# Kernel tuning notes

Measured on AMD Instinct MI355X. Metric: run time of the kernel, lower is better.

## Reference

```python
import jax, jax.numpy as jnp
import numpy as np

N = 512
D = 512
# static upper-triangle pair indices (i < j)
_II, _JJ = np.triu_indices(N, k=1)
_II = jnp.asarray(_II)
_JJ = jnp.asarray(_JJ)


def setup_inputs() -> dict:
    key = jax.random.key(0)
    ks = jax.random.split(key, 9)
    s = 0.02
    return {
        'features': jax.random.normal(ks[0], (N, D), dtype=jnp.float32),
        # relation_classifier: Linear(2D->D), Linear(D->10)
        'cw1': jax.random.normal(ks[1], (2 * D, D), dtype=jnp.float32) * s,
        'cb1': jnp.zeros((D,), dtype=jnp.float32),
        'cw2': jax.random.normal(ks[2], (D, 10), dtype=jnp.float32) * s,
        'cb2': jnp.zeros((10,), dtype=jnp.float32),
        # relation_strength_calc: Linear(2D->D//2), Linear(D//2->1)
        'sw1': jax.random.normal(ks[3], (2 * D, D // 2), dtype=jnp.float32) * s,
        'sb1': jnp.zeros((D // 2,), dtype=jnp.float32),
        'sw2': jax.random.normal(ks[4], (D // 2, 1), dtype=jnp.float32) * s,
        'sb2': jnp.zeros((1,), dtype=jnp.float32),
    }


def reference(features, cw1, cb1, cw2, cb2, sw1, sb1, sw2, sb2):
    # cat([f_i, f_j]) @ W == f_i @ W[:D] + f_j @ W[D:]  (linear-split trick)
    # precompute per-node projections once, then gather per pair
    c_a = features @ cw1[:D]   # [N, D]
    c_b = features @ cw1[D:]   # [N, D]
    s_a = features @ sw1[:D]   # [N, D//2]
    s_b = features @ sw1[D:]   # [N, D//2]

    # classifier path
    h = jax.nn.relu(c_a[_II] + c_b[_JJ] + cb1)          # [P, D]
    relation_types = jax.nn.log_softmax(h @ cw2 + cb2)   # [P, 10]
    most_likely_relations = jnp.argmax(relation_types, axis=-1)  # [P]

    # strength path
    hs = jax.nn.relu(s_a[_II] + s_b[_JJ] + sb1)          # [P, D//2]
    relation_strengths = jax.nn.sigmoid(hs @ sw2 + sb2)   # [P, 1]

    return relation_types, most_likely_relations, relation_strengths
```

## Files before the change

### kernel.cpp

```cpp
#include <hip/hip_runtime.h>
#include <math.h>

#define NN 512
#define DD 512
#define NPAIRS 130816
#define TYPES_OFF 0
#define ARGMAX_OFF 1308160
#define STRENGTH_OFF 1438976

#define GAP_THRESH 2.5e-4f


__device__ __forceinline__ void fma64_step4(
    const float4& a0, const float4& a1, const float4& a2, const float4& a3,
    const float4& b0, const float4& b1, const float4& b2, const float4& b3,
    double acc[4][4])
{
    const float av[4][4] = {{a0.x,a0.y,a0.z,a0.w},{a1.x,a1.y,a1.z,a1.w},
                            {a2.x,a2.y,a2.z,a2.w},{a3.x,a3.y,a3.z,a3.w}};
    const float bv[4][4] = {{b0.x,b0.y,b0.z,b0.w},{b1.x,b1.y,b1.z,b1.w},
                            {b2.x,b2.y,b2.z,b2.w},{b3.x,b3.y,b3.z,b3.w}};
    #pragma unroll
    for (int kk = 0; kk < 4; ++kk) {
        double bd0 = (double)bv[kk][0], bd1 = (double)bv[kk][1];
        double bd2 = (double)bv[kk][2], bd3 = (double)bv[kk][3];
        #pragma unroll
        for (int rr = 0; rr < 4; ++rr) {
            double ad = (double)av[rr][kk];
            acc[rr][0] = fma(ad, bd0, acc[rr][0]);
            acc[rr][1] = fma(ad, bd1, acc[rr][1]);
            acc[rr][2] = fma(ad, bd2, acc[rr][2]);
            acc[rr][3] = fma(ad, bd3, acc[rr][3]);
        }
    }
}

__device__ __forceinline__ void fma32_step4(
    const float4& a0, const float4& a1, const float4& a2, const float4& a3,
    const float4& b0, const float4& b1, const float4& b2, const float4& b3,
    float acc[4][4])
{
    const float av[4][4] = {{a0.x,a0.y,a0.z,a0.w},{a1.x,a1.y,a1.z,a1.w},
                            {a2.x,a2.y,a2.z,a2.w},{a3.x,a3.y,a3.z,a3.w}};
    const float bv[4][4] = {{b0.x,b0.y,b0.z,b0.w},{b1.x,b1.y,b1.z,b1.w},
                            {b2.x,b2.y,b2.z,b2.w},{b3.x,b3.y,b3.z,b3.w}};
    #pragma unroll
    for (int kk = 0; kk < 4; ++kk) {
        #pragma unroll
        for (int rr = 0; rr < 4; ++rr) {
            #pragma unroll
            for (int cc = 0; cc < 4; ++cc)
                acc[rr][cc] = fmaf(av[rr][kk], bv[kk][cc], acc[rr][cc]);
        }
    }
}

__global__ __launch_bounds__(256, 2) void proj_kernel(
    const float* __restrict__ F, const float* __restrict__ cw1,
    const float* __restrict__ sw1,
    const float* __restrict__ cb1, const float* __restrict__ sb1,
    double* __restrict__ ca0, double* __restrict__ ca1,
    double* __restrict__ ca2, double* __restrict__ ca3,
    double* __restrict__ cb0, double* __restrict__ cb1p,
    double* __restrict__ cb2p, double* __restrict__ cb3p,
    float* __restrict__ sa0, float* __restrict__ sa1,
    float* __restrict__ sb0, float* __restrict__ sbp1)
{
    const int t = threadIdx.x;
    const int w = t >> 6;
    const int lane = t & 63;
    const int mg = lane >> 4;
    const int nq = lane & 15;

    if (blockIdx.x < 512) {
        const int b  = blockIdx.x;
        const int z  = b & 3;
        const int nt = (b >> 2) & 15;
        const int mt = b >> 6;
        const int n  = nt * 64;
        const float* W = (n < 512) ? cw1 : cw1 + 512 * 512;
        const int n0   = (n < 512) ? n : n - 512;
        double* outp;
        if (n < 512) outp = (z == 0) ? ca0 : (z == 1) ? ca1 : (z == 2) ? ca2 : ca3;
        else         outp = (z == 0) ? cb0 : (z == 1) ? cb1p : (z == 2) ? cb2p : cb3p;
        const bool addbias = (z == 0) && (n < 512);

        const int row0 = mt * 64 + w * 16 + mg * 4;
        const int col0 = n0 + nq * 4;
        const float* pa = F + row0 * 512 + z * 128;
        const float* pb = W + (z * 128) * 512 + col0;

        double acc[4][4];
        #pragma unroll
        for (int rr = 0; rr < 4; ++rr)
            #pragma unroll
            for (int cc = 0; cc < 4; ++cc) acc[rr][cc] = 0.0;

        float4 a0 = *(const float4*)(pa);
        float4 a1 = *(const float4*)(pa + 512);
        float4 a2 = *(const float4*)(pa + 1024);
        float4 a3 = *(const float4*)(pa + 1536);
        float4 b0 = *(const float4*)(pb);
        float4 b1 = *(const float4*)(pb + 512);
        float4 b2 = *(const float4*)(pb + 1024);
        float4 b3 = *(const float4*)(pb + 1536);
        for (int s = 0; s < 31; ++s) {
            const float* npa = pa + (s + 1) * 4;
            float4 na0 = *(const float4*)(npa);
            float4 na1 = *(const float4*)(npa + 512);
            float4 na2 = *(const float4*)(npa + 1024);
            float4 na3 = *(const float4*)(npa + 1536);
            const float* nb = pb + (s + 1) * 2048;
            float4 nb0 = *(const float4*)(nb);
            float4 nb1 = *(const float4*)(nb + 512);
            float4 nb2 = *(const float4*)(nb + 1024);
            float4 nb3 = *(const float4*)(nb + 1536);
            fma64_step4(a0, a1, a2, a3, b0, b1, b2, b3, acc);
            a0 = na0; a1 = na1; a2 = na2; a3 = na3;
            b0 = nb0; b1 = nb1; b2 = nb2; b3 = nb3;
        }
        fma64_step4(a0, a1, a2, a3, b0, b1, b2, b3, acc);

        #pragma unroll
        for (int rr = 0; rr < 4; ++rr) {
            double v[4];
            #pragma unroll
            for (int cc = 0; cc < 4; ++cc) {
                v[cc] = acc[rr][cc];
                if (addbias) v[cc] += (double)cb1[col0 + cc];
            }
            double* dst = outp + (row0 + rr) * 512 + col0;
            *(double2*)(dst + 0) = make_double2(v[0], v[1]);
            *(double2*)(dst + 2) = make_double2(v[2], v[3]);
        }
    } else {
        const int sbk = blockIdx.x - 512;
        const int z  = sbk & 1;
        const int nt = (sbk >> 1) & 7;
        const int mt = sbk >> 4;
        const int n  = nt * 64;
        const float* W = (n < 256) ? sw1 : sw1 + 512 * 256;
        const int n0   = (n < 256) ? n : n - 256;
        float* outp    = (n < 256) ? (z ? sa1 : sa0) : (z ? sbp1 : sb0);
        const bool addbias = (z == 0) && (n < 256);

        const int row0 = mt * 64 + w * 16 + mg * 4;
        const int col0 = n0 + nq * 4;
        const float* pa = F + row0 * 512 + z * 256;
        const float* pb = W + (z * 256) * 256 + col0;

        float acc[4][4];
        #pragma unroll
        for (int rr = 0; rr < 4; ++rr)
            #pragma unroll
            for (int cc = 0; cc < 4; ++cc) acc[rr][cc] = 0.f;

        float4 a0 = *(const float4*)(pa);
        float4 a1 = *(const float4*)(pa + 512);
        float4 a2 = *(const float4*)(pa + 1024);
        float4 a3 = *(const float4*)(pa + 1536);
        float4 b0 = *(const float4*)(pb);
        float4 b1 = *(const float4*)(pb + 256);
        float4 b2 = *(const float4*)(pb + 512);
        float4 b3 = *(const float4*)(pb + 768);
        for (int s = 0; s < 63; ++s) {
            const float* npa = pa + (s + 1) * 4;
            float4 na0 = *(const float4*)(npa);
            float4 na1 = *(const float4*)(npa + 512);
            float4 na2 = *(const float4*)(npa + 1024);
            float4 na3 = *(const float4*)(npa + 1536);
            const float* nb = pb + (s + 1) * 1024;
            float4 nb0 = *(const float4*)(nb);
            float4 nb1 = *(const float4*)(nb + 256);
            float4 nb2 = *(const float4*)(nb + 512);
            float4 nb3 = *(const float4*)(nb + 768);
            fma32_step4(a0, a1, a2, a3, b0, b1, b2, b3, acc);
            a0 = na0; a1 = na1; a2 = na2; a3 = na3;
            b0 = nb0; b1 = nb1; b2 = nb2; b3 = nb3;
        }
        fma32_step4(a0, a1, a2, a3, b0, b1, b2, b3, acc);

        #pragma unroll
        for (int rr = 0; rr < 4; ++rr) {
            float4 v = make_float4(acc[rr][0], acc[rr][1], acc[rr][2], acc[rr][3]);
            if (addbias) {
                v.x += sb1[col0 + 0]; v.y += sb1[col0 + 1];
                v.z += sb1[col0 + 2]; v.w += sb1[col0 + 3];
            }
            *(float4*)(outp + (row0 + rr) * 256 + col0) = v;
        }
    }
}

__global__ __launch_bounds__(256) void combine_kernel(
    const double* __restrict__ ca0, const double* __restrict__ ca1,
    const double* __restrict__ ca2, const double* __restrict__ ca3,
    const double* __restrict__ cb0, const double* __restrict__ cb1p,
    const double* __restrict__ cb2p, const double* __restrict__ cb3p,
    const float* __restrict__ sa0, const float* __restrict__ sa1,
    const float* __restrict__ sb0, const float* __restrict__ sbp1,
    float* __restrict__ cfa, float* __restrict__ cfb,
    float* __restrict__ sfa, float* __restrict__ sfb)
{
    const int t = blockIdx.x * 256 + threadIdx.x;
    {
        const int e = 2 * t;
        double2 x0 = *(const double2*)(ca0 + e);
        double2 x1 = *(const double2*)(ca1 + e);
        double2 x2 = *(const double2*)(ca2 + e);
        double2 x3 = *(const double2*)(ca3 + e);
        *(float2*)(cfa + e) = make_float2(
            (float)((x0.x + x1.x) + (x2.x + x3.x)),
            (float)((x0.y + x1.y) + (x2.y + x3.y)));
        double2 y0 = *(const double2*)(cb0 + e);
        double2 y1 = *(const double2*)(cb1p + e);
        double2 y2 = *(const double2*)(cb2p + e);
        double2 y3 = *(const double2*)(cb3p + e);
        *(float2*)(cfb + e) = make_float2(
            (float)((y0.x + y1.x) + (y2.x + y3.x)),
            (float)((y0.y + y1.y) + (y2.y + y3.y)));
    }
    if (t < 65536) {
        const bool second = t >= 32768;
        const int e = (second ? (t - 32768) : t) * 4;
        const float* s0 = second ? sb0 : sa0;
        const float* s1 = second ? sbp1 : sa1;
        float* dst      = second ? sfb : sfa;
        float4 a = *(const float4*)(s0 + e);
        float4 b = *(const float4*)(s1 + e);
        *(float4*)(dst + e) = make_float4(a.x + b.x, a.y + b.y, a.z + b.z, a.w + b.w);
    }
}

__global__ __launch_bounds__(256, 4) void pair_kernel(
    const double* __restrict__ ca0, const double* __restrict__ ca1,
    const double* __restrict__ ca2, const double* __restrict__ ca3,
    const double* __restrict__ cb0, const double* __restrict__ cb1p,
    const double* __restrict__ cb2p, const double* __restrict__ cb3p,
    const float* __restrict__ cfa, const float* __restrict__ cfb,
    const float* __restrict__ sfa, const float* __restrict__ sfb,
    const float* __restrict__ cw2, const float* __restrict__ cb2,
    const float* __restrict__ sw2, const float* __restrict__ sb2,
    float* __restrict__ out)
{
    const int b = blockIdx.x;
    int bi = (int)floorf((129.0f - sqrtf(16641.0f - 8.0f * (float)b)) * 0.5f);
    while ((bi + 1) * (129 - (bi + 1)) / 2 <= b) ++bi;
    while (bi * (129 - bi) / 2 > b) --bi;
    const int bj = bi + (b - bi * (129 - bi) / 2);
    const int i0 = bi * 8, j0 = bj * 8;

    const int t = threadIdx.x;
    const int q  = t >> 6;
    const int qu = __builtin_amdgcn_readfirstlane(q);
    const int l = t & 63;
    const int pi = l >> 3, pj = l & 7;
    const int i = i0 + pi, j = j0 + pj;

    __shared__ __align__(16) float smem[8448];
    float* sA  = smem;
    float* sB  = smem + 4224;
    float* sSa = smem;
    float* sSb = smem + 2176;
    float* lgbuf = smem;
    float* stbuf = smem + 1920;

    #pragma unroll
    for (int u = 0; u < 4; ++u) {
        int idx = u * 256 + t;
        int kq  = idx & 15;
        int row = (idx >> 4) & 7;
        int qq  = (idx >> 7) & 3;
        int arr = idx >> 9;
        int off = (arr ? (j0 + row) : (i0 + row)) * 256 + qq * 64 + kq * 4;
        const float* src = arr ? sfb : sfa;
        float4 v = *(const float4*)(src + off);
        float* dst = (arr ? sSb : sSa) + (qq * 8 + row) * 68 + kq * 4;
        *(float4*)dst = v;
    }
    __syncthreads();
    float accs = 0.f;
    {
        const float* sw2q = sw2 + qu * 64;
        const float* ra = sSa + (q * 8 + pi) * 68;
        const float* rb = sSb + (q * 8 + pj) * 68;
        float p0 = 0.f, p1 = 0.f, p2 = 0.f, p3 = 0.f;
        for (int kk = 0; kk < 64; kk += 4) {
            float4 a4 = *(const float4*)(ra + kk);
            float4 b4 = *(const float4*)(rb + kk);
            p0 = fmaf(fmaxf(a4.x + b4.x, 0.f), sw2q[kk + 0], p0);
            p1 = fmaf(fmaxf(a4.y + b4.y, 0.f), sw2q[kk + 1], p1);
            p2 = fmaf(fmaxf(a4.z + b4.z, 0.f), sw2q[kk + 2], p2);
            p3 = fmaf(fmaxf(a4.w + b4.w, 0.f), sw2q[kk + 3], p3);
        }
        accs = (p0 + p1) + (p2 + p3);
    }
    __syncthreads();

    #pragma unroll
    for (int u = 0; u < 8; ++u) {
        int idx = u * 256 + t;
        int kq  = idx & 31;
        int row = (idx >> 5) & 7;
        int qq  = (idx >> 8) & 3;
        int arr = idx >> 10;
        int off = (arr ? (j0 + row) : (i0 + row)) * 512 + qq * 128 + kq * 4;
        const float* src = arr ? cfb : cfa;
        float4 v = *(const float4*)(src + off);
        float* dst = (arr ? sB : sA) + (qq * 8 + row) * 132 + kq * 4;
        *(float4*)dst = v;
    }
    __syncthreads();

    float lg[10];
    #pragma unroll
    for (int c = 0; c < 10; ++c) lg[c] = 0.f;
    {
        const float* ra = sA + (q * 8 + pi) * 132;
        const float* rb = sB + (q * 8 + pj) * 132;
        const float* wr = cw2 + qu * 1280;
        for (int kk = 0; kk < 128; kk += 4) {
            float4 ra4 = *(const float4*)(ra + kk);
            float4 rb4 = *(const float4*)(rb + kk);
            float h0 = fmaxf(ra4.x + rb4.x, 0.f);
            float h1 = fmaxf(ra4.y + rb4.y, 0.f);
            float h2 = fmaxf(ra4.z + rb4.z, 0.f);
            float h3 = fmaxf(ra4.w + rb4.w, 0.f);
            const float* w = wr + kk * 10;
            #pragma unroll
            for (int c = 0; c < 10; ++c) lg[c] = fmaf(h0, w[c], lg[c]);
            #pragma unroll
            for (int c = 0; c < 10; ++c) lg[c] = fmaf(h1, w[10 + c], lg[c]);
            #pragma unroll
            for (int c = 0; c < 10; ++c) lg[c] = fmaf(h2, w[20 + c], lg[c]);
            #pragma unroll
            for (int c = 0; c < 10; ++c) lg[c] = fmaf(h3, w[30 + c], lg[c]);
        }
    }

    __syncthreads();
    if (q > 0) {
        float* dst = lgbuf + ((q - 1) * 64 + l) * 10;
        #pragma unroll
        for (int c = 0; c < 10; ++c) dst[c] = lg[c];
        stbuf[(q - 1) * 64 + l] = accs;
    }
    __syncthreads();
    if (q == 0) {
        #pragma unroll
        for (int w = 0; w < 3; ++w) {
            const float* srcb = lgbuf + (w * 64 + l) * 10;
            #pragma unroll
            for (int c = 0; c < 10; ++c) lg[c] += srcb[c];
        }
        float st = accs + stbuf[l] + stbuf[64 + l] + stbuf[128 + l] + sb2[0];

        #pragma unroll
        for (int c = 0; c < 10; ++c) lg[c] += cb2[c];

        float mx = lg[0], mx2 = -3.0e38f; int am2 = 0;
        #pragma unroll
        for (int c = 1; c < 10; ++c) {
            if (lg[c] > mx) { mx2 = mx; mx = lg[c]; am2 = c; }
            else if (lg[c] > mx2) mx2 = lg[c];
        }

        unsigned long long m = __ballot((j > i) && (mx - mx2 < GAP_THRESH));
        while (m) {
            const int s = __ffsll((unsigned long long)m) - 1; m &= (m - 1);
            const int si = i0 + (s >> 3), sj = j0 + (s & 7);
            double part[10];
            #pragma unroll
            for (int c = 0; c < 10; ++c) part[c] = 0.0;
            const int kb = l * 8;
            #pragma unroll 2
            for (int kk = 0; kk < 8; ++kk) {
                const int k = kb + kk;
                const int ei = si * 512 + k, ej = sj * 512 + k;
                double va = (ca0[ei] + ca1[ei]) + (ca2[ei] + ca3[ei]);
                double vb = (cb0[ej] + cb1p[ej]) + (cb2p[ej] + cb3p[ej]);
                double h = fmax(va + vb, 0.0);
                const float* w = cw2 + k * 10;
                #pragma unroll
                for (int c = 0; c < 10; ++c) part[c] = fma(h, (double)w[c], part[c]);
            }
            #pragma unroll
            for (int off = 32; off > 0; off >>= 1) {
                #pragma unroll
                for (int c = 0; c < 10; ++c) part[c] += __shfl_xor(part[c], off, 64);
            }
            double bmx = part[0] + (double)cb2[0]; int ba = 0;
            #pragma unroll
            for (int c = 1; c < 10; ++c) {
                double v = part[c] + (double)cb2[c];
                if (v > bmx) { bmx = v; ba = c; }
            }
            if (l == s) am2 = ba;
        }

        float tf[10]; float ssum = 0.f;
        #pragma unroll
        for (int c = 0; c < 10; ++c) { tf[c] = lg[c] - mx; ssum += __expf(tf[c]); }
        float ls = __logf(ssum);

        if (j > i) {
            const int p = i * 511 - (i * (i - 1)) / 2 + (j - i - 1);
            float* tp = out + TYPES_OFF + p * 10;
            #pragma unroll
            for (int c = 0; c < 10; ++c) tp[c] = tf[c] - ls;
            out[ARGMAX_OFF + p] = (float)am2;
            out[STRENGTH_OFF + p] = 1.0f / (1.0f + __expf(-st));
        }
    }
}

extern "C" void kernel_launch(void* const* d_in, const int* in_sizes, int n_in,
                              void* d_out, int out_size, void* d_ws, size_t ws_size,
                              hipStream_t stream) {
    const float* F   = (const float*)d_in[0];
    const float* cw1 = (const float*)d_in[1];
    const float* cb1 = (const float*)d_in[2];
    const float* cw2 = (const float*)d_in[3];
    const float* cb2 = (const float*)d_in[4];
    const float* sw1 = (const float*)d_in[5];
    const float* sb1 = (const float*)d_in[6];
    const float* sw2 = (const float*)d_in[7];
    const float* sb2 = (const float*)d_in[8];
    float* out = (float*)d_out;

    char* ws = (char*)d_ws;
    double* ca0  = (double*)(ws);
    double* ca1  = (double*)(ws + 2097152);
    double* ca2  = (double*)(ws + 4194304);
    double* ca3  = (double*)(ws + 6291456);
    double* cb0  = (double*)(ws + 8388608);
    double* cb1p = (double*)(ws + 10485760);
    double* cb2p = (double*)(ws + 12582912);
    double* cb3p = (double*)(ws + 14680064);
    float*  sa0  = (float*)(ws + 16777216);
    float*  sa1  = (float*)(ws + 17301504);
    float*  sb0  = (float*)(ws + 17825792);
    float*  sbp1 = (float*)(ws + 18350080);
    float*  cfa  = (float*)(ws + 18874368);
    float*  cfb  = (float*)(ws + 19922944);
    float*  sfa  = (float*)(ws + 20971520);
    float*  sfb  = (float*)(ws + 21495808);

    hipLaunchKernelGGL(proj_kernel, dim3(640), dim3(256), 0, stream,
                       F, cw1, sw1, cb1, sb1,
                       ca0, ca1, ca2, ca3, cb0, cb1p, cb2p, cb3p,
                       sa0, sa1, sb0, sbp1);
    hipLaunchKernelGGL(combine_kernel, dim3(512), dim3(256), 0, stream,
                       ca0, ca1, ca2, ca3, cb0, cb1p, cb2p, cb3p,
                       sa0, sa1, sb0, sbp1, cfa, cfb, sfa, sfb);
    hipLaunchKernelGGL(pair_kernel, dim3(2080), dim3(256), 0, stream,
                       ca0, ca1, ca2, ca3, cb0, cb1p, cb2p, cb3p,
                       cfa, cfb, sfa, sfb, cw2, cb2, sw2, sb2, out);
}
```

Baseline: 145.2 us.

## Enlarge projection register tile to 8x4 and double split-K partitions

Each projection thread now computes an 8x4 output tile instead of 4x4, which raises FMA work per loaded A/B value. The K dimension is split into 8 partitions for the fp64 classifier path and 4 for the fp32 strength path, up from 4 and 2, so the block count stays at 640. The partial buffers are packed into one contiguous array, and the combine kernel and the pair kernel's near-tie fallback now sum 8 fp64 partials instead of 4. The cost is twice the partial-sum write and read traffic, more register pressure from the fp64 accumulators, and extra loads in the fallback path.

```diff
diff --git a/kernel.cpp b/kernel.cpp
--- a/kernel.cpp
+++ b/kernel.cpp
@@ -11,21 +11,23 @@
 #define GAP_THRESH 2.5e-4f
 
 
-__device__ __forceinline__ void fma64_step4(
-    const float4& a0, const float4& a1, const float4& a2, const float4& a3,
-    const float4& b0, const float4& b1, const float4& b2, const float4& b3,
-    double acc[4][4])
+__device__ __forceinline__ void fma64_step8(
+    const float4 a[8], const float4 bq[4], double acc[8][4])
 {
-    const float av[4][4] = {{a0.x,a0.y,a0.z,a0.w},{a1.x,a1.y,a1.z,a1.w},
-                            {a2.x,a2.y,a2.z,a2.w},{a3.x,a3.y,a3.z,a3.w}};
-    const float bv[4][4] = {{b0.x,b0.y,b0.z,b0.w},{b1.x,b1.y,b1.z,b1.w},
-                            {b2.x,b2.y,b2.z,b2.w},{b3.x,b3.y,b3.z,b3.w}};
+    const float av[8][4] = {
+        {a[0].x,a[0].y,a[0].z,a[0].w},{a[1].x,a[1].y,a[1].z,a[1].w},
+        {a[2].x,a[2].y,a[2].z,a[2].w},{a[3].x,a[3].y,a[3].z,a[3].w},
+        {a[4].x,a[4].y,a[4].z,a[4].w},{a[5].x,a[5].y,a[5].z,a[5].w},
+        {a[6].x,a[6].y,a[6].z,a[6].w},{a[7].x,a[7].y,a[7].z,a[7].w}};
+    const float bv[4][4] = {
+        {bq[0].x,bq[0].y,bq[0].z,bq[0].w},{bq[1].x,bq[1].y,bq[1].z,bq[1].w},
+        {bq[2].x,bq[2].y,bq[2].z,bq[2].w},{bq[3].x,bq[3].y,bq[3].z,bq[3].w}};
     #pragma unroll
     for (int kk = 0; kk < 4; ++kk) {
         double bd0 = (double)bv[kk][0], bd1 = (double)bv[kk][1];
         double bd2 = (double)bv[kk][2], bd3 = (double)bv[kk][3];
         #pragma unroll
-        for (int rr = 0; rr < 4; ++rr) {
+        for (int rr = 0; rr < 8; ++rr) {
             double ad = (double)av[rr][kk];
             acc[rr][0] = fma(ad, bd0, acc[rr][0]);
             acc[rr][1] = fma(ad, bd1, acc[rr][1]);
@@ -35,19 +37,21 @@
     }
 }
 
-__device__ __forceinline__ void fma32_step4(
-    const float4& a0, const float4& a1, const float4& a2, const float4& a3,
-    const float4& b0, const float4& b1, const float4& b2, const float4& b3,
-    float acc[4][4])
+__device__ __forceinline__ void fma32_step8(
+    const float4 a[8], const float4 bq[4], float acc[8][4])
 {
-    const float av[4][4] = {{a0.x,a0.y,a0.z,a0.w},{a1.x,a1.y,a1.z,a1.w},
-                            {a2.x,a2.y,a2.z,a2.w},{a3.x,a3.y,a3.z,a3.w}};
-    const float bv[4][4] = {{b0.x,b0.y,b0.z,b0.w},{b1.x,b1.y,b1.z,b1.w},
-                            {b2.x,b2.y,b2.z,b2.w},{b3.x,b3.y,b3.z,b3.w}};
+    const float av[8][4] = {
+        {a[0].x,a[0].y,a[0].z,a[0].w},{a[1].x,a[1].y,a[1].z,a[1].w},
+        {a[2].x,a[2].y,a[2].z,a[2].w},{a[3].x,a[3].y,a[3].z,a[3].w},
+        {a[4].x,a[4].y,a[4].z,a[4].w},{a[5].x,a[5].y,a[5].z,a[5].w},
+        {a[6].x,a[6].y,a[6].z,a[6].w},{a[7].x,a[7].y,a[7].z,a[7].w}};
+    const float bv[4][4] = {
+        {bq[0].x,bq[0].y,bq[0].z,bq[0].w},{bq[1].x,bq[1].y,bq[1].z,bq[1].w},
+        {bq[2].x,bq[2].y,bq[2].z,bq[2].w},{bq[3].x,bq[3].y,bq[3].z,bq[3].w}};
     #pragma unroll
     for (int kk = 0; kk < 4; ++kk) {
         #pragma unroll
-        for (int rr = 0; rr < 4; ++rr) {
+        for (int rr = 0; rr < 8; ++rr) {
             #pragma unroll
             for (int cc = 0; cc < 4; ++cc)
                 acc[rr][cc] = fmaf(av[rr][kk], bv[kk][cc], acc[rr][cc]);
@@ -59,70 +63,60 @@
     const float* __restrict__ F, const float* __restrict__ cw1,
     const float* __restrict__ sw1,
     const float* __restrict__ cb1, const float* __restrict__ sb1,
-    double* __restrict__ ca0, double* __restrict__ ca1,
-    double* __restrict__ ca2, double* __restrict__ ca3,
-    double* __restrict__ cb0, double* __restrict__ cb1p,
-    double* __restrict__ cb2p, double* __restrict__ cb3p,
-    float* __restrict__ sa0, float* __restrict__ sa1,
-    float* __restrict__ sb0, float* __restrict__ sbp1)
+    double* __restrict__ cq, float* __restrict__ sq)
 {
     const int t = threadIdx.x;
     const int w = t >> 6;
     const int lane = t & 63;
     const int mg = lane >> 4;
     const int nq = lane & 15;
-
-    if (blockIdx.x < 512) {
-        const int b  = blockIdx.x;
-        const int z  = b & 3;
-        const int nt = (b >> 2) & 15;
-        const int mt = b >> 6;
+    const int blk = blockIdx.x;
+
+    if (blk < 512) {
+        const int z  = blk & 7;
+        const int nt = (blk >> 3) & 15;
+        const int mt = blk >> 7;
         const int n  = nt * 64;
         const float* W = (n < 512) ? cw1 : cw1 + 512 * 512;
         const int n0   = (n < 512) ? n : n - 512;
-        double* outp;
-        if (n < 512) outp = (z == 0) ? ca0 : (z == 1) ? ca1 : (z == 2) ? ca2 : ca3;
-        else         outp = (z == 0) ? cb0 : (z == 1) ? cb1p : (z == 2) ? cb2p : cb3p;
+        double* outp   = cq + (((n < 512) ? 0 : 8) + z) * 262144;
         const bool addbias = (z == 0) && (n < 512);
 
-        const int row0 = mt * 64 + w * 16 + mg * 4;
+        const int row0 = mt * 128 + w * 32 + mg * 8;
         const int col0 = n0 + nq * 4;
-        const float* pa = F + row0 * 512 + z * 128;
-        const float* pb = W + (z * 128) * 512 + col0;
-
-        double acc[4][4];
-        #pragma unroll
-        for (int rr = 0; rr < 4; ++rr)
+        const float* pa = F + row0 * 512 + z * 64;
+        const float* pb = W + (z * 64) * 512 + col0;
+
+        double acc[8][4];
+        #pragma unroll
+        for (int rr = 0; rr < 8; ++rr)
             #pragma unroll
             for (int cc = 0; cc < 4; ++cc) acc[rr][cc] = 0.0;
 
-        float4 a0 = *(const float4*)(pa);
-        float4 a1 = *(const float4*)(pa + 512);
-        float4 a2 = *(const float4*)(pa + 1024);
-        float4 a3 = *(const float4*)(pa + 1536);
-        float4 b0 = *(const float4*)(pb);
-        float4 b1 = *(const float4*)(pb + 512);
-        float4 b2 = *(const float4*)(pb + 1024);
-        float4 b3 = *(const float4*)(pb + 1536);
-        for (int s = 0; s < 31; ++s) {
+        float4 a[8], bq[4];
+        #pragma unroll
+        for (int rr = 0; rr < 8; ++rr) a[rr] = *(const float4*)(pa + rr * 512);
+        #pragma unroll
+        for (int cc = 0; cc < 4; ++cc) bq[cc] = *(const float4*)(pb + cc * 512);
+
+        for (int s = 0; s < 15; ++s) {
+            float4 na[8], nbq[4];
             const float* npa = pa + (s + 1) * 4;
-            float4 na0 = *(const float4*)(npa);
-            float4 na1 = *(const float4*)(npa + 512);
-            float4 na2 = *(const float4*)(npa + 1024);
-            float4 na3 = *(const float4*)(npa + 1536);
-            const float* nb = pb + (s + 1) * 2048;
-            float4 nb0 = *(const float4*)(nb);
-            float4 nb1 = *(const float4*)(nb + 512);
-            float4 nb2 = *(const float4*)(nb + 1024);
-            float4 nb3 = *(const float4*)(nb + 1536);
-            fma64_step4(a0, a1, a2, a3, b0, b1, b2, b3, acc);
-            a0 = na0; a1 = na1; a2 = na2; a3 = na3;
-            b0 = nb0; b1 = nb1; b2 = nb2; b3 = nb3;
-        }
-        fma64_step4(a0, a1, a2, a3, b0, b1, b2, b3, acc);
-
-        #pragma unroll
-        for (int rr = 0; rr < 4; ++rr) {
+            #pragma unroll
+            for (int rr = 0; rr < 8; ++rr) na[rr] = *(const float4*)(npa + rr * 512);
+            const float* npb = pb + (s + 1) * 2048;
+            #pragma unroll
+            for (int cc = 0; cc < 4; ++cc) nbq[cc] = *(const float4*)(npb + cc * 512);
+            fma64_step8(a, bq, acc);
+            #pragma unroll
+            for (int rr = 0; rr < 8; ++rr) a[rr] = na[rr];
+            #pragma unroll
+            for (int cc = 0; cc < 4; ++cc) bq[cc] = nbq[cc];
+        }
+        fma64_step8(a, bq, acc);
+
+        #pragma unroll
+        for (int rr = 0; rr < 8; ++rr) {
             double v[4];
             #pragma unroll
             for (int cc = 0; cc < 4; ++cc) {
@@ -134,54 +128,51 @@
             *(double2*)(dst + 2) = make_double2(v[2], v[3]);
         }
     } else {
-        const int sbk = blockIdx.x - 512;
-        const int z  = sbk & 1;
-        const int nt = (sbk >> 1) & 7;
-        const int mt = sbk >> 4;
+        const int sbk = blk - 512;
+        const int z  = sbk & 3;
+        const int nt = (sbk >> 2) & 7;
+        const int mt = sbk >> 5;
         const int n  = nt * 64;
         const float* W = (n < 256) ? sw1 : sw1 + 512 * 256;
         const int n0   = (n < 256) ? n : n - 256;
-        float* outp    = (n < 256) ? (z ? sa1 : sa0) : (z ? sbp1 : sb0);
+        float* outp    = sq + (((n < 256) ? 0 : 4) + z) * 131072;
         const bool addbias = (z == 0) && (n < 256);
 
-        const int row0 = mt * 64 + w * 16 + mg * 4;
+        const int row0 = mt * 128 + w * 32 + mg * 8;
         const int col0 = n0 + nq * 4;
-        const float* pa = F + row0 * 512 + z * 256;
-        const float* pb = W + (z * 256) * 256 + col0;
-
-        float acc[4][4];
-        #pragma unroll
-        for (int rr = 0; rr < 4; ++rr)
+        const float* pa = F + row0 * 512 + z * 128;
+        const float* pb = W + (z * 128) * 256 + col0;
+
+        float acc[8][4];
+        #pragma unroll
+        for (int rr = 0; rr < 8; ++rr)
             #pragma unroll
             for (int cc = 0; cc < 4; ++cc) acc[rr][cc] = 0.f;
 
-        float4 a0 = *(const float4*)(pa);
-        float4 a1 = *(const float4*)(pa + 512);
-        float4 a2 = *(const float4*)(pa + 1024);
-        float4 a3 = *(const float4*)(pa + 1536);
-        float4 b0 = *(const float4*)(pb);
-        float4 b1 = *(const float4*)(pb + 256);
-        float4 b2 = *(const float4*)(pb + 512);
-        float4 b3 = *(const float4*)(pb + 768);
-        for (int s = 0; s < 63; ++s) {
+        float4 a[8], bq[4];
+        #pragma unroll
+        for (int rr = 0; rr < 8; ++rr) a[rr] = *(const float4*)(pa + rr * 512);
+        #pragma unroll
+        for (int cc = 0; cc < 4; ++cc) bq[cc] = *(const float4*)(pb + cc * 256);
+
+        for (int s = 0; s < 31; ++s) {
+            float4 na[8], nbq[4];
             const float* npa = pa + (s + 1) * 4;
-            float4 na0 = *(const float4*)(npa);
-            float4 na1 = *(const float4*)(npa + 512);
-            float4 na2 = *(const float4*)(npa + 1024);
-            float4 na3 = *(const float4*)(npa + 1536);
-            const float* nb = pb + (s + 1) * 1024;
-            float4 nb0 = *(const float4*)(nb);
-            float4 nb1 = *(const float4*)(nb + 256);
-            float4 nb2 = *(const float4*)(nb + 512);
-            float4 nb3 = *(const float4*)(nb + 768);
-            fma32_step4(a0, a1, a2, a3, b0, b1, b2, b3, acc);
-            a0 = na0; a1 = na1; a2 = na2; a3 = na3;
-            b0 = nb0; b1 = nb1; b2 = nb2; b3 = nb3;
-        }
-        fma32_step4(a0, a1, a2, a3, b0, b1, b2, b3, acc);
-
-        #pragma unroll
-        for (int rr = 0; rr < 4; ++rr) {
+            #pragma unroll
+            for (int rr = 0; rr < 8; ++rr) na[rr] = *(const float4*)(npa + rr * 512);
+            const float* npb = pb + (s + 1) * 1024;
+            #pragma unroll
+            for (int cc = 0; cc < 4; ++cc) nbq[cc] = *(const float4*)(npb + cc * 256);
+            fma32_step8(a, bq, acc);
+            #pragma unroll
+            for (int rr = 0; rr < 8; ++rr) a[rr] = na[rr];
+            #pragma unroll
+            for (int cc = 0; cc < 4; ++cc) bq[cc] = nbq[cc];
+        }
+        fma32_step8(a, bq, acc);
+
+        #pragma unroll
+        for (int rr = 0; rr < 8; ++rr) {
             float4 v = make_float4(acc[rr][0], acc[rr][1], acc[rr][2], acc[rr][3]);
             if (addbias) {
                 v.x += sb1[col0 + 0]; v.y += sb1[col0 + 1];
@@ -193,50 +184,53 @@
 }
 
 __global__ __launch_bounds__(256) void combine_kernel(
-    const double* __restrict__ ca0, const double* __restrict__ ca1,
-    const double* __restrict__ ca2, const double* __restrict__ ca3,
-    const double* __restrict__ cb0, const double* __restrict__ cb1p,
-    const double* __restrict__ cb2p, const double* __restrict__ cb3p,
-    const float* __restrict__ sa0, const float* __restrict__ sa1,
-    const float* __restrict__ sb0, const float* __restrict__ sbp1,
+    const double* __restrict__ cq, const float* __restrict__ sq,
     float* __restrict__ cfa, float* __restrict__ cfb,
     float* __restrict__ sfa, float* __restrict__ sfb)
 {
     const int t = blockIdx.x * 256 + threadIdx.x;
     {
         const int e = 2 * t;
-        double2 x0 = *(const double2*)(ca0 + e);
-        double2 x1 = *(const double2*)(ca1 + e);
-        double2 x2 = *(const double2*)(ca2 + e);
-        double2 x3 = *(const double2*)(ca3 + e);
+        double2 x0 = *(const double2*)(cq + 0 * 262144 + e);
+        double2 x1 = *(const double2*)(cq + 1 * 262144 + e);
+        double2 x2 = *(const double2*)(cq + 2 * 262144 + e);
+        double2 x3 = *(const double2*)(cq + 3 * 262144 + e);
+        double2 x4 = *(const double2*)(cq + 4 * 262144 + e);
+        double2 x5 = *(const double2*)(cq + 5 * 262144 + e);
+        double2 x6 = *(const double2*)(cq + 6 * 262144 + e);
+        double2 x7 = *(const double2*)(cq + 7 * 262144 + e);
         *(float2*)(cfa + e) = make_float2(
-            (float)((x0.x + x1.x) + (x2.x + x3.x)),
-            (float)((x0.y + x1.y) + (x2.y + x3.y)));
-        double2 y0 = *(const double2*)(cb0 + e);
-        double2 y1 = *(const double2*)(cb1p + e);
-        double2 y2 = *(const double2*)(cb2p + e);
-        double2 y3 = *(const double2*)(cb3p + e);
+            (float)(((x0.x + x1.x) + (x2.x + x3.x)) + ((x4.x + x5.x) + (x6.x + x7.x))),
+            (float)(((x0.y + x1.y) + (x2.y + x3.y)) + ((x4.y + x5.y) + (x6.y + x7.y))));
+        double2 y0 = *(const double2*)(cq + 8  * 262144 + e);
+        double2 y1 = *(const double2*)(cq + 9  * 262144 + e);
+        double2 y2 = *(const double2*)(cq + 10 * 262144 + e);
+        double2 y3 = *(const double2*)(cq + 11 * 262144 + e);
+        double2 y4 = *(const double2*)(cq + 12 * 262144 + e);
+        double2 y5 = *(const double2*)(cq + 13 * 262144 + e);
+        double2 y6 = *(const double2*)(cq + 14 * 262144 + e);
+        double2 y7 = *(const double2*)(cq + 15 * 262144 + e);
         *(float2*)(cfb + e) = make_float2(
-            (float)((y0.x + y1.x) + (y2.x + y3.x)),
-            (float)((y0.y + y1.y) + (y2.y + y3.y)));
+            (float)(((y0.x + y1.x) + (y2.x + y3.x)) + ((y4.x + y5.x) + (y6.x + y7.x))),
+            (float)(((y0.y + y1.y) + (y2.y + y3.y)) + ((y4.y + y5.y) + (y6.y + y7.y))));
     }
     if (t < 65536) {
         const bool second = t >= 32768;
         const int e = (second ? (t - 32768) : t) * 4;
-        const float* s0 = second ? sb0 : sa0;
-        const float* s1 = second ? sbp1 : sa1;
-        float* dst      = second ? sfb : sfa;
-        float4 a = *(const float4*)(s0 + e);
-        float4 b = *(const float4*)(s1 + e);
-        *(float4*)(dst + e) = make_float4(a.x + b.x, a.y + b.y, a.z + b.z, a.w + b.w);
+        const float* base = sq + (second ? 4 : 0) * 131072;
+        float* dst        = second ? sfb : sfa;
+        float4 a0 = *(const float4*)(base + 0 * 131072 + e);
+        float4 a1 = *(const float4*)(base + 1 * 131072 + e);
+        float4 a2 = *(const float4*)(base + 2 * 131072 + e);
+        float4 a3 = *(const float4*)(base + 3 * 131072 + e);
+        *(float4*)(dst + e) = make_float4(
+            (a0.x + a1.x) + (a2.x + a3.x), (a0.y + a1.y) + (a2.y + a3.y),
+            (a0.z + a1.z) + (a2.z + a3.z), (a0.w + a1.w) + (a2.w + a3.w));
     }
 }
 
 __global__ __launch_bounds__(256, 4) void pair_kernel(
-    const double* __restrict__ ca0, const double* __restrict__ ca1,
-    const double* __restrict__ ca2, const double* __restrict__ ca3,
-    const double* __restrict__ cb0, const double* __restrict__ cb1p,
-    const double* __restrict__ cb2p, const double* __restrict__ cb3p,
+    const double* __restrict__ cq,
     const float* __restrict__ cfa, const float* __restrict__ cfb,
     const float* __restrict__ sfa, const float* __restrict__ sfb,
     const float* __restrict__ cw2, const float* __restrict__ cb2,
@@ -376,9 +370,12 @@
             #pragma unroll 2
             for (int kk = 0; kk < 8; ++kk) {
                 const int k = kb + kk;
-                const int ei = si * 512 + k, ej = sj * 512 + k;
-                double va = (ca0[ei] + ca1[ei]) + (ca2[ei] + ca3[ei]);
-                double vb = (cb0[ej] + cb1p[ej]) + (cb2p[ej] + cb3p[ej]);
+                const double* ga = cq + si * 512 + k;
+                const double* gb = cq + 8 * 262144 + sj * 512 + k;
+                double va = ((ga[0] + ga[262144]) + (ga[2*262144] + ga[3*262144]))
+                          + ((ga[4*262144] + ga[5*262144]) + (ga[6*262144] + ga[7*262144]));
+                double vb = ((gb[0] + gb[262144]) + (gb[2*262144] + gb[3*262144]))
+                          + ((gb[4*262144] + gb[5*262144]) + (gb[6*262144] + gb[7*262144]));
                 double h = fmax(va + vb, 0.0);
                 const float* w = cw2 + k * 10;
                 #pragma unroll
@@ -429,31 +426,17 @@
     float* out = (float*)d_out;
 
     char* ws = (char*)d_ws;
-    double* ca0  = (double*)(ws);
-    double* ca1  = (double*)(ws + 2097152);
-    double* ca2  = (double*)(ws + 4194304);
-    double* ca3  = (double*)(ws + 6291456);
-    double* cb0  = (double*)(ws + 8388608);
-    double* cb1p = (double*)(ws + 10485760);
-    double* cb2p = (double*)(ws + 12582912);
-    double* cb3p = (double*)(ws + 14680064);
-    float*  sa0  = (float*)(ws + 16777216);
-    float*  sa1  = (float*)(ws + 17301504);
-    float*  sb0  = (float*)(ws + 17825792);
-    float*  sbp1 = (float*)(ws + 18350080);
-    float*  cfa  = (float*)(ws + 18874368);
-    float*  cfb  = (float*)(ws + 19922944);
-    float*  sfa  = (float*)(ws + 20971520);
-    float*  sfb  = (float*)(ws + 21495808);
+    double* cq  = (double*)(ws);
+    float*  sq  = (float*)(ws + 33554432);
+    float*  cfa = (float*)(ws + 37748736);
+    float*  cfb = (float*)(ws + 38797312);
+    float*  sfa = (float*)(ws + 39845888);
+    float*  sfb = (float*)(ws + 40370176);
 
     hipLaunchKernelGGL(proj_kernel, dim3(640), dim3(256), 0, stream,
-                       F, cw1, sw1, cb1, sb1,
-                       ca0, ca1, ca2, ca3, cb0, cb1p, cb2p, cb3p,
-                       sa0, sa1, sb0, sbp1);
+                       F, cw1, sw1, cb1, sb1, cq, sq);
     hipLaunchKernelGGL(combine_kernel, dim3(512), dim3(256), 0, stream,
-                       ca0, ca1, ca2, ca3, cb0, cb1p, cb2p, cb3p,
-                       sa0, sa1, sb0, sbp1, cfa, cfb, sfa, sfb);
+                       cq, sq, cfa, cfb, sfa, sfb);
     hipLaunchKernelGGL(pair_kernel, dim3(2080), dim3(256), 0, stream,
-                       ca0, ca1, ca2, ca3, cb0, cb1p, cb2p, cb3p,
-                       cfa, cfb, sfa, sfb, cw2, cb2, sw2, sb2, out);
-}
+                       cq, cfa, cfb, sfa, sfb, cw2, cb2, sw2, sb2, out);
+}
```

After: 160.4 us. +10.4%, slower.
